# Kernel optimization log

Hardware: AMD Instinct MI355X
Metric: run time of the kernel (lower is better)

Reference implementation:

```python
import jax, jax.numpy as jnp
import numpy as np

N = 100000
E = 1600000
IN_DIM = 64
HID = 64
OUT = 64
BN_EPS = 1e-5


def setup_inputs() -> dict:
    key = jax.random.key(0)
    ks = jax.random.split(key, 16)
    x = jax.random.normal(ks[0], (N, IN_DIM), dtype=jnp.float32)
    edge_index = jax.random.randint(ks[1], (2, E), 0, N, dtype=jnp.int64)
    def lin(k, fan_in, fan_out):
        bound = 1.0 / np.sqrt(fan_in)
        kw, kb = jax.random.split(k)
        W = jax.random.uniform(kw, (fan_in, fan_out), jnp.float32, -bound, bound)
        b = jax.random.uniform(kb, (fan_out,), jnp.float32, -bound, bound)
        return W, b
    W1, b1 = lin(ks[2], IN_DIM, HID)
    W2, b2 = lin(ks[3], HID, HID)
    g1 = jnp.ones((HID,), jnp.float32)
    bt1 = jnp.zeros((HID,), jnp.float32)
    eps1 = jnp.zeros((), jnp.float32)
    W3, b3 = lin(ks[4], HID, HID)
    W4, b4 = lin(ks[5], HID, OUT)
    g2 = jnp.ones((OUT,), jnp.float32)
    bt2 = jnp.zeros((OUT,), jnp.float32)
    eps2 = jnp.zeros((), jnp.float32)
    return {"x": x, "edge_index": edge_index,
            "W1": W1, "b1": b1, "W2": W2, "b2": b2, "g1": g1, "bt1": bt1, "eps1": eps1,
            "W3": W3, "b3": b3, "W4": W4, "b4": b4, "g2": g2, "bt2": bt2, "eps2": eps2}


def _bn(h, gamma, beta):
    # BatchNorm1d in training mode: per-feature batch stats, biased variance
    mean = jnp.mean(h, axis=0)
    var = jnp.mean((h - mean) ** 2, axis=0)
    return (h - mean) * jax.lax.rsqrt(var + BN_EPS) * gamma + beta


def _gin_conv(x, src, dst, eps, Wa, ba, Wb, bb, gamma, beta):
    # scatter-add aggregation: sum_{j in N(i)} x_j
    agg = jax.ops.segment_sum(x[src], dst, num_segments=N)  # [N, D]
    h = (1.0 + eps) * x + agg
    h = jax.nn.relu(h @ Wa + ba)
    h = jax.nn.relu(h @ Wb + bb)
    return _bn(h, gamma, beta)


def reference(x, edge_index, W1, b1, W2, b2, g1, bt1, eps1, W3, b3, W4, b4, g2, bt2, eps2):
    src, dst = edge_index[0], edge_index[1]
    h = _gin_conv(x, src, dst, eps1, W1, b1, W2, b2, g1, bt1)
    h = _gin_conv(h, src, dst, eps2, W3, b3, W4, b4, g2, bt2)
    return (h, jax.nn.log_softmax(h, axis=-1))
```

## Files before the change

### kernel.cpp

```cpp
#include <hip/hip_runtime.h>

#define NN 100000
#define NE 1600000
#define NB 256
#define BSZ 391
#define EB 782

typedef __attribute__((ext_vector_type(8))) short short8;
typedef __attribute__((ext_vector_type(4))) float floatx4;

__device__ __forceinline__ unsigned short f2bf(float f) {
  unsigned u = __float_as_uint(f);
  u += 0x7fffu + ((u >> 16) & 1u);
  return (unsigned short)(u >> 16);
}
__device__ __forceinline__ float bf2f(unsigned short b) {
  return __uint_as_float(((unsigned)b) << 16);
}

__global__ __launch_bounds__(256) void k_cvtW(const float* __restrict__ W1,
                                              const float* __restrict__ W2,
                                              const float* __restrict__ W3,
                                              const float* __restrict__ W4,
                                              unsigned short* __restrict__ Wb) {
  int i = blockIdx.x * 256 + threadIdx.x;
  Wb[i] = f2bf(W1[i]);
  Wb[4096 + i] = f2bf(W2[i]);
  Wb[8192 + i] = f2bf(W3[i]);
  Wb[12288 + i] = f2bf(W4[i]);
}

__global__ __launch_bounds__(256) void k_phist(const int* __restrict__ dst,
                                               int* __restrict__ blockHist) {
  __shared__ int h[NB];
  h[threadIdx.x] = 0;
  __syncthreads();
  int base = blockIdx.x * 2048;
#pragma unroll
  for (int i = 0; i < 8; i++) {
    int e = base + i * 256 + threadIdx.x;
    if (e < NE) atomicAdd(&h[dst[e] / BSZ], 1);
  }
  __syncthreads();
  blockHist[blockIdx.x * NB + threadIdx.x] = h[threadIdx.x];
}

__global__ __launch_bounds__(1024) void k_colscan(const int* __restrict__ blockHist,
                                                  int* __restrict__ offsL,
                                                  int* __restrict__ colTot) {
  __shared__ int sh[1024];
  int c = blockIdx.x, t = threadIdx.x;
  int v = (t < EB) ? blockHist[t * NB + c] : 0;
  sh[t] = v;
  __syncthreads();
  for (int off = 1; off < 1024; off <<= 1) {
    int u = (t >= off) ? sh[t - off] : 0;
    __syncthreads();
    sh[t] += u;
    __syncthreads();
  }
  if (t < EB) offsL[t * NB + c] = sh[t] - v;
  if (t == EB - 1) colTot[c] = sh[t];
}

__global__ __launch_bounds__(256) void k_basescan(const int* __restrict__ colTot,
                                                  int* __restrict__ base) {
  __shared__ int sh[256];
  int t = threadIdx.x;
  int v = colTot[t];
  sh[t] = v;
  __syncthreads();
  for (int off = 1; off < 256; off <<= 1) {
    int u = (t >= off) ? sh[t - off] : 0;
    __syncthreads();
    sh[t] += u;
    __syncthreads();
  }
  base[t] = sh[t] - v;
  if (t == 255) base[256] = sh[255];
}

__global__ __launch_bounds__(256) void k_escat(const int* __restrict__ src,
                                               const int* __restrict__ dst,
                                               const int* __restrict__ offsL,
                                               const int* __restrict__ base,
                                               int2* __restrict__ ed) {
  __shared__ int h[NB];
  h[threadIdx.x] = 0;
  __syncthreads();
  int eb = blockIdx.x * 2048;
  const int* ofs = offsL + blockIdx.x * NB;
#pragma unroll
  for (int i = 0; i < 8; i++) {
    int e = eb + i * 256 + threadIdx.x;
    if (e < NE) {
      int d = dst[e];
      int c = d / BSZ;
      int r = atomicAdd(&h[c], 1);
      ed[base[c] + ofs[c] + r] = make_int2(src[e], d);
    }
  }
}

__global__ __launch_bounds__(256) void k_ellfill(const int2* __restrict__ ed,
                                                 const int* __restrict__ base,
                                                 int* __restrict__ ell,
                                                 int* __restrict__ deg) {
  __shared__ int cur[BSZ];
  int c = blockIdx.x;
  for (int i = threadIdx.x; i < BSZ; i += 256) cur[i] = 0;
  __syncthreads();
  int lo = base[c], hi = base[c + 1];
  int n0 = c * BSZ;
  for (int e = lo + threadIdx.x; e < hi; e += 256) {
    int2 sd = ed[e];
    int slot = atomicAdd(&cur[sd.y - n0], 1);
    if (slot < 64) ell[sd.y * 64 + slot] = sd.x;
  }
  __syncthreads();
  for (int i = threadIdx.x; i < BSZ; i += 256) {
    int n = n0 + i;
    if (n < NN) deg[n] = min(cur[i], 64);
  }
}

template <int MODE>
__global__ __launch_bounds__(256) void k_gather(const float* __restrict__ xf,
                                                const unsigned short* __restrict__ xb,
                                                const int* __restrict__ deg,
                                                const int* __restrict__ ell,
                                                const float* __restrict__ eps,
                                                const float* __restrict__ AB,
                                                unsigned short* __restrict__ agg) {
  const int lane = threadIdx.x & 31;
  const int slot = threadIdx.x >> 5;
  const int n = blockIdx.x * 8 + slot;
  const int fo = 2 * lane;
  float A0 = 1.0f, B0 = 0.0f, A1 = 1.0f, B1 = 0.0f;
  if (MODE) { A0 = AB[fo]; B0 = AB[64 + fo]; A1 = AB[fo + 1]; B1 = AB[64 + fo + 1]; }
  float s0, s1;
  if (MODE) {
    ushort2 u = *(const ushort2*)(xb + n * 64 + fo);
    s0 = fmaf(bf2f(u.x), A0, B0);
    s1 = fmaf(bf2f(u.y), A1, B1);
  } else {
    float2 u = *(const float2*)(xf + n * 64 + fo);
    s0 = u.x;
    s1 = u.y;
  }
  const float es = 1.0f + eps[0];
  float a0 = es * s0, a1 = es * s1;
  float b0 = 0, b1 = 0, c0 = 0, c1 = 0, d0 = 0, d1 = 0;
  const int cnt = deg[n];
  const int* row = ell + n * 64;
  const int4* r4 = (const int4*)row;
  int j = 0;
  for (; j + 4 <= cnt; j += 4) {
    int4 s4 = r4[j >> 2];
    if (MODE) {
      ushort2 u0 = *(const ushort2*)(xb + s4.x * 64 + fo);
      ushort2 u1 = *(const ushort2*)(xb + s4.y * 64 + fo);
      ushort2 u2 = *(const ushort2*)(xb + s4.z * 64 + fo);
      ushort2 u3 = *(const ushort2*)(xb + s4.w * 64 + fo);
      a0 = fmaf(bf2f(u0.x), A0, a0); a1 = fmaf(bf2f(u0.y), A1, a1);
      b0 = fmaf(bf2f(u1.x), A0, b0); b1 = fmaf(bf2f(u1.y), A1, b1);
      c0 = fmaf(bf2f(u2.x), A0, c0); c1 = fmaf(bf2f(u2.y), A1, c1);
      d0 = fmaf(bf2f(u3.x), A0, d0); d1 = fmaf(bf2f(u3.y), A1, d1);
      a0 += B0; a1 += B1; b0 += B0; b1 += B1;
      c0 += B0; c1 += B1; d0 += B0; d1 += B1;
    } else {
      float2 u0 = *(const float2*)(xf + s4.x * 64 + fo);
      float2 u1 = *(const float2*)(xf + s4.y * 64 + fo);
      float2 u2 = *(const float2*)(xf + s4.z * 64 + fo);
      float2 u3 = *(const float2*)(xf + s4.w * 64 + fo);
      a0 += u0.x; a1 += u0.y;
      b0 += u1.x; b1 += u1.y;
      c0 += u2.x; c1 += u2.y;
      d0 += u3.x; d1 += u3.y;
    }
  }
  for (; j < cnt; j++) {
    int s = row[j];
    if (MODE) {
      ushort2 u = *(const ushort2*)(xb + s * 64 + fo);
      a0 += fmaf(bf2f(u.x), A0, B0);
      a1 += fmaf(bf2f(u.y), A1, B1);
    } else {
      float2 u = *(const float2*)(xf + s * 64 + fo);
      a0 += u.x;
      a1 += u.y;
    }
  }
  float r0 = (a0 + b0) + (c0 + d0);
  float r1 = (a1 + b1) + (c1 + d1);
  ushort2 st;
  st.x = f2bf(r0);
  st.y = f2bf(r1);
  *(ushort2*)(agg + n * 64 + fo) = st;
}

__global__ __launch_bounds__(256) void k_mlp_mfma(
    const unsigned short* __restrict__ agg, const unsigned short* __restrict__ Wab,
    const float* __restrict__ ba, const float* __restrict__ bb,
    unsigned short* __restrict__ h2, double* __restrict__ stats) {
  const int l = threadIdx.x & 63;
  const int wv = threadIdx.x >> 6;
  const int l16 = l & 15, quad = l >> 4;

  short8 wfa[4][2], wfb[4][2];
#pragma unroll
  for (int c = 0; c < 4; c++)
#pragma unroll
    for (int t = 0; t < 2; t++)
#pragma unroll
      for (int j = 0; j < 8; j++) {
        int k = t * 32 + quad * 8 + j, nn = c * 16 + l16;
        wfa[c][t][j] = (short)Wab[k * 64 + nn];
        wfb[c][t][j] = (short)Wab[4096 + k * 64 + nn];
      }
  float bia[4], bib[4];
#pragma unroll
  for (int c = 0; c < 4; c++) { bia[c] = ba[c * 16 + l16]; bib[c] = bb[c * 16 + l16]; }

  __shared__ float Hs[4][16][68];
  __shared__ float sS[4][64], sQ[4][64];
  float ssum[4] = {0, 0, 0, 0}, ssq[4] = {0, 0, 0, 0};

  const int totw = gridDim.x * 4;
  for (int tile = blockIdx.x * 4 + wv; tile < NN / 16; tile += totw) {
    const int r0 = tile * 16;
    const unsigned short* ap = agg + (r0 + l16) * 64 + quad * 8;
    short8 a0 = *(const short8*)ap;
    short8 a1 = *(const short8*)(ap + 32);
#pragma unroll
    for (int c = 0; c < 4; c++) {
      floatx4 acc = {0.f, 0.f, 0.f, 0.f};
      acc = __builtin_amdgcn_mfma_f32_16x16x32_bf16(a0, wfa[c][0], acc, 0, 0, 0);
      acc = __builtin_amdgcn_mfma_f32_16x16x32_bf16(a1, wfa[c][1], acc, 0, 0, 0);
#pragma unroll
      for (int r = 0; r < 4; r++)
        Hs[wv][quad * 4 + r][c * 16 + l16] = fmaxf(acc[r] + bia[c], 0.0f);
    }
    short8 a20, a21;
#pragma unroll
    for (int j = 0; j < 8; j++) {
      a20[j] = (short)f2bf(Hs[wv][l16][quad * 8 + j]);
      a21[j] = (short)f2bf(Hs[wv][l16][32 + quad * 8 + j]);
    }
#pragma unroll
    for (int c = 0; c < 4; c++) {
      floatx4 acc = {0.f, 0.f, 0.f, 0.f};
      acc = __builtin_amdgcn_mfma_f32_16x16x32_bf16(a20, wfb[c][0], acc, 0, 0, 0);
      acc = __builtin_amdgcn_mfma_f32_16x16x32_bf16(a21, wfb[c][1], acc, 0, 0, 0);
#pragma unroll
      for (int r = 0; r < 4; r++) {
        float v = fmaxf(acc[r] + bib[c], 0.0f);
        h2[(r0 + quad * 4 + r) * 64 + c * 16 + l16] = f2bf(v);
        ssum[c] += v;
        ssq[c] += v * v;
      }
    }
  }
#pragma unroll
  for (int c = 0; c < 4; c++) {
    float s = ssum[c], q = ssq[c];
    s += __shfl_xor(s, 16, 64); s += __shfl_xor(s, 32, 64);
    q += __shfl_xor(q, 16, 64); q += __shfl_xor(q, 32, 64);
    if (quad == 0) { sS[wv][c * 16 + l16] = s; sQ[wv][c * 16 + l16] = q; }
  }
  __syncthreads();
  if (threadIdx.x < 64) {
    int ff = threadIdx.x;
    float s = sS[0][ff] + sS[1][ff] + sS[2][ff] + sS[3][ff];
    float q = sQ[0][ff] + sQ[1][ff] + sQ[2][ff] + sQ[3][ff];
    unsafeAtomicAdd(&stats[ff], (double)s);
    unsafeAtomicAdd(&stats[64 + ff], (double)q);
  }
}

__global__ void k_bnfin(const double* __restrict__ stats, const float* __restrict__ gam,
                        const float* __restrict__ bet, float* __restrict__ AB) {
  int f = threadIdx.x;
  double mean = stats[f] * (1.0 / NN);
  double var = stats[64 + f] * (1.0 / NN) - mean * mean;
  if (var < 0.0) var = 0.0;
  float rstd = (float)(1.0 / sqrt(var + 1e-5));
  float A = gam[f] * rstd;
  float B = bet[f] - (float)mean * A;
  AB[f] = A;
  AB[64 + f] = B;
}

__global__ __launch_bounds__(256) void k_out(const unsigned short* __restrict__ h2,
                                             const float* __restrict__ AB,
                                             float* __restrict__ out) {
  int f = threadIdx.x & 63;
  int n = blockIdx.x * 4 + (threadIdx.x >> 6);
  float v = bf2f(h2[n * 64 + f]);
  float h = fmaf(v, AB[f], AB[64 + f]);
  float m = h;
#pragma unroll
  for (int off = 32; off; off >>= 1) m = fmaxf(m, __shfl_xor(m, off, 64));
  float e = expf(h - m);
  float ssum = e;
#pragma unroll
  for (int off = 32; off; off >>= 1) ssum += __shfl_xor(ssum, off, 64);
  float lsm = (h - m) - logf(ssum);
  out[n * 64 + f] = h;
  out[(size_t)NN * 64 + n * 64 + f] = lsm;
}

extern "C" void kernel_launch(void* const* d_in, const int* in_sizes, int n_in,
                              void* d_out, int out_size, void* d_ws, size_t ws_size,
                              hipStream_t stream) {
  const float* x = (const float*)d_in[0];
  const int* ei = (const int*)d_in[1];
  const float* W1 = (const float*)d_in[2];
  const float* b1 = (const float*)d_in[3];
  const float* W2 = (const float*)d_in[4];
  const float* b2 = (const float*)d_in[5];
  const float* g1 = (const float*)d_in[6];
  const float* bt1 = (const float*)d_in[7];
  const float* e1 = (const float*)d_in[8];
  const float* W3 = (const float*)d_in[9];
  const float* b3 = (const float*)d_in[10];
  const float* W4 = (const float*)d_in[11];
  const float* b4 = (const float*)d_in[12];
  const float* g2 = (const float*)d_in[13];
  const float* bt2 = (const float*)d_in[14];
  const float* e2 = (const float*)d_in[15];
  const int* src = ei;
  const int* dst = ei + NE;

  char* ws = (char*)d_ws;
  unsigned short* aggb = (unsigned short*)(ws);
  unsigned short* h2b = (unsigned short*)(ws + 12800000);
  int* ell = (int*)(ws + 25600000);
  int2* ed = (int2*)(ws + 51200000);
  int* blockHist = (int*)(ws + 64000000);
  int* offsL = (int*)(ws + 64800768);
  int* colTot = (int*)(ws + 65601536);
  int* base = (int*)(ws + 65602560);
  int* deg = (int*)(ws + 65603600);
  double* st1 = (double*)(ws + 66003600);
  double* st2 = (double*)(ws + 66004624);
  float* AB1 = (float*)(ws + 66005648);
  float* AB2 = (float*)(ws + 66006160);
  unsigned short* Wbb = (unsigned short*)(ws + 66006672);
  float* out = (float*)d_out;

  hipMemsetAsync(ws + 66003600, 0, 2048, stream);

  k_cvtW<<<16, 256, 0, stream>>>(W1, W2, W3, W4, Wbb);

  k_phist<<<EB, 256, 0, stream>>>(dst, blockHist);
  k_colscan<<<NB, 1024, 0, stream>>>(blockHist, offsL, colTot);
  k_basescan<<<1, 256, 0, stream>>>(colTot, base);
  k_escat<<<EB, 256, 0, stream>>>(src, dst, offsL, base, ed);
  k_ellfill<<<NB, 256, 0, stream>>>(ed, base, ell, deg);

  k_gather<0><<<NN / 8, 256, 0, stream>>>(x, nullptr, deg, ell, e1, nullptr, aggb);
  k_mlp_mfma<<<391, 256, 0, stream>>>(aggb, Wbb, b1, b2, h2b, st1);
  k_bnfin<<<1, 64, 0, stream>>>(st1, g1, bt1, AB1);
  k_gather<1><<<NN / 8, 256, 0, stream>>>(nullptr, h2b, deg, ell, e2, AB1, aggb);
  k_mlp_mfma<<<391, 256, 0, stream>>>(aggb, Wbb + 8192, b3, b4, h2b, st2);
  k_bnfin<<<1, 64, 0, stream>>>(st2, g2, bt2, AB2);
  k_out<<<NN / 4, 256, 0, stream>>>(h2b, AB2, out);
}
```

Measured before the change: 314.0 us.

## Slice features into 8-wide column blocks and transpose ELL for cache-local gathers

Node features, aggregates and hidden activations are stored as 8 slices of 8 features each ([slice][node][8]). The gather kernel now uses one thread per node per slice, and reads neighbor indices from a transposed ELL table so those index loads coalesce across threads. Because each slice pass only touches a few MB of feature data, the random neighbor reads should mostly hit L2 or MALL instead of DRAM. The BatchNorm affine of layer one is folded algebraically into a single FMA at the end of the gather, and the MLP grid is doubled. The costs are an extra transpose kernel for x, reading each neighbor list eight times, and small 16–32 byte random accesses that may waste cache-line bandwidth.

```diff
diff --git a/kernel.cpp b/kernel.cpp
--- a/kernel.cpp
+++ b/kernel.cpp
@@ -104,7 +104,7 @@
 
 __global__ __launch_bounds__(256) void k_ellfill(const int2* __restrict__ ed,
                                                  const int* __restrict__ base,
-                                                 int* __restrict__ ell,
+                                                 int* __restrict__ ellT,
                                                  int* __restrict__ deg) {
   __shared__ int cur[BSZ];
   int c = blockIdx.x;
@@ -115,7 +115,7 @@
   for (int e = lo + threadIdx.x; e < hi; e += 256) {
     int2 sd = ed[e];
     int slot = atomicAdd(&cur[sd.y - n0], 1);
-    if (slot < 64) ell[sd.y * 64 + slot] = sd.x;
+    if (slot < 64) ellT[(size_t)slot * NN + sd.y] = sd.x;
   }
   __syncthreads();
   for (int i = threadIdx.x; i < BSZ; i += 256) {
@@ -124,79 +124,117 @@
   }
 }
 
+__global__ __launch_bounds__(256) void k_xpose(const float* __restrict__ x,
+                                               float* __restrict__ xs) {
+  int nl = threadIdx.x >> 3, s = threadIdx.x & 7;
+  int n = blockIdx.x * 32 + nl;
+  const floatx4* rp = (const floatx4*)(x + (size_t)n * 64 + s * 8);
+  floatx4 v0 = rp[0], v1 = rp[1];
+  floatx4* wp = (floatx4*)(xs + ((size_t)s * NN + n) * 8);
+  __builtin_nontemporal_store(v0, wp);
+  __builtin_nontemporal_store(v1, wp + 1);
+}
+
 template <int MODE>
-__global__ __launch_bounds__(256) void k_gather(const float* __restrict__ xf,
+__global__ __launch_bounds__(256) void k_gather(const float* __restrict__ xs,
                                                 const unsigned short* __restrict__ xb,
                                                 const int* __restrict__ deg,
-                                                const int* __restrict__ ell,
+                                                const int* __restrict__ ellT,
                                                 const float* __restrict__ eps,
                                                 const float* __restrict__ AB,
                                                 unsigned short* __restrict__ agg) {
-  const int lane = threadIdx.x & 31;
-  const int slot = threadIdx.x >> 5;
-  const int n = blockIdx.x * 8 + slot;
-  const int fo = 2 * lane;
-  float A0 = 1.0f, B0 = 0.0f, A1 = 1.0f, B1 = 0.0f;
-  if (MODE) { A0 = AB[fo]; B0 = AB[64 + fo]; A1 = AB[fo + 1]; B1 = AB[64 + fo + 1]; }
-  float s0, s1;
+  const int s = blockIdx.x & 7;
+  const int n = (blockIdx.x >> 3) * 256 + (int)threadIdx.x;
+  if (n >= NN) return;
+  const float es = 1.0f + eps[0];
+  const int cnt = __builtin_nontemporal_load(deg + n);
+  const size_t sbase = (size_t)s * NN;
+
+  float a0[8], a1[8];
+#pragma unroll
+  for (int i = 0; i < 8; i++) a1[i] = 0.0f;
+
   if (MODE) {
-    ushort2 u = *(const ushort2*)(xb + n * 64 + fo);
-    s0 = fmaf(bf2f(u.x), A0, B0);
-    s1 = fmaf(bf2f(u.y), A1, B1);
+    short8 v = *(const short8*)(xb + (sbase + n) * 8);
+#pragma unroll
+    for (int i = 0; i < 8; i++) a0[i] = es * bf2f((unsigned short)v[i]);
   } else {
-    float2 u = *(const float2*)(xf + n * 64 + fo);
-    s0 = u.x;
-    s1 = u.y;
-  }
-  const float es = 1.0f + eps[0];
-  float a0 = es * s0, a1 = es * s1;
-  float b0 = 0, b1 = 0, c0 = 0, c1 = 0, d0 = 0, d1 = 0;
-  const int cnt = deg[n];
-  const int* row = ell + n * 64;
-  const int4* r4 = (const int4*)row;
+    const floatx4* sp = (const floatx4*)(xs + (sbase + n) * 8);
+    floatx4 v0 = sp[0], v1 = sp[1];
+    a0[0] = es * v0.x; a0[1] = es * v0.y; a0[2] = es * v0.z; a0[3] = es * v0.w;
+    a0[4] = es * v1.x; a0[5] = es * v1.y; a0[6] = es * v1.z; a0[7] = es * v1.w;
+  }
+
+  const int* ep = ellT + n;
   int j = 0;
   for (; j + 4 <= cnt; j += 4) {
-    int4 s4 = r4[j >> 2];
+    int i0 = __builtin_nontemporal_load(ep + (size_t)(j + 0) * NN);
+    int i1 = __builtin_nontemporal_load(ep + (size_t)(j + 1) * NN);
+    int i2 = __builtin_nontemporal_load(ep + (size_t)(j + 2) * NN);
+    int i3 = __builtin_nontemporal_load(ep + (size_t)(j + 3) * NN);
     if (MODE) {
-      ushort2 u0 = *(const ushort2*)(xb + s4.x * 64 + fo);
-      ushort2 u1 = *(const ushort2*)(xb + s4.y * 64 + fo);
-      ushort2 u2 = *(const ushort2*)(xb + s4.z * 64 + fo);
-      ushort2 u3 = *(const ushort2*)(xb + s4.w * 64 + fo);
-      a0 = fmaf(bf2f(u0.x), A0, a0); a1 = fmaf(bf2f(u0.y), A1, a1);
-      b0 = fmaf(bf2f(u1.x), A0, b0); b1 = fmaf(bf2f(u1.y), A1, b1);
-      c0 = fmaf(bf2f(u2.x), A0, c0); c1 = fmaf(bf2f(u2.y), A1, c1);
-      d0 = fmaf(bf2f(u3.x), A0, d0); d1 = fmaf(bf2f(u3.y), A1, d1);
-      a0 += B0; a1 += B1; b0 += B0; b1 += B1;
-      c0 += B0; c1 += B1; d0 += B0; d1 += B1;
+      short8 u0 = *(const short8*)(xb + (sbase + i0) * 8);
+      short8 u1 = *(const short8*)(xb + (sbase + i1) * 8);
+      short8 u2 = *(const short8*)(xb + (sbase + i2) * 8);
+      short8 u3 = *(const short8*)(xb + (sbase + i3) * 8);
+#pragma unroll
+      for (int i = 0; i < 8; i++) {
+        a0[i] += bf2f((unsigned short)u0[i]) + bf2f((unsigned short)u1[i]);
+        a1[i] += bf2f((unsigned short)u2[i]) + bf2f((unsigned short)u3[i]);
+      }
     } else {
-      float2 u0 = *(const float2*)(xf + s4.x * 64 + fo);
-      float2 u1 = *(const float2*)(xf + s4.y * 64 + fo);
-      float2 u2 = *(const float2*)(xf + s4.z * 64 + fo);
-      float2 u3 = *(const float2*)(xf + s4.w * 64 + fo);
-      a0 += u0.x; a1 += u0.y;
-      b0 += u1.x; b1 += u1.y;
-      c0 += u2.x; c1 += u2.y;
-      d0 += u3.x; d1 += u3.y;
+      const floatx4* p0 = (const floatx4*)(xs + (sbase + i0) * 8);
+      const floatx4* p1 = (const floatx4*)(xs + (sbase + i1) * 8);
+      const floatx4* p2 = (const floatx4*)(xs + (sbase + i2) * 8);
+      const floatx4* p3 = (const floatx4*)(xs + (sbase + i3) * 8);
+      floatx4 q00 = p0[0], q01 = p0[1], q10 = p1[0], q11 = p1[1];
+      floatx4 q20 = p2[0], q21 = p2[1], q30 = p3[0], q31 = p3[1];
+      a0[0] += q00.x + q10.x; a0[1] += q00.y + q10.y;
+      a0[2] += q00.z + q10.z; a0[3] += q00.w + q10.w;
+      a0[4] += q01.x + q11.x; a0[5] += q01.y + q11.y;
+      a0[6] += q01.z + q11.z; a0[7] += q01.w + q11.w;
+      a1[0] += q20.x + q30.x; a1[1] += q20.y + q30.y;
+      a1[2] += q20.z + q30.z; a1[3] += q20.w + q30.w;
+      a1[4] += q21.x + q31.x; a1[5] += q21.y + q31.y;
+      a1[6] += q21.z + q31.z; a1[7] += q21.w + q31.w;
     }
   }
   for (; j < cnt; j++) {
-    int s = row[j];
+    int i0 = __builtin_nontemporal_load(ep + (size_t)j * NN);
     if (MODE) {
-      ushort2 u = *(const ushort2*)(xb + s * 64 + fo);
-      a0 += fmaf(bf2f(u.x), A0, B0);
-      a1 += fmaf(bf2f(u.y), A1, B1);
+      short8 u0 = *(const short8*)(xb + (sbase + i0) * 8);
+#pragma unroll
+      for (int i = 0; i < 8; i++) a0[i] += bf2f((unsigned short)u0[i]);
     } else {
-      float2 u = *(const float2*)(xf + s * 64 + fo);
-      a0 += u.x;
-      a1 += u.y;
-    }
-  }
-  float r0 = (a0 + b0) + (c0 + d0);
-  float r1 = (a1 + b1) + (c1 + d1);
-  ushort2 st;
-  st.x = f2bf(r0);
-  st.y = f2bf(r1);
-  *(ushort2*)(agg + n * 64 + fo) = st;
+      const floatx4* p0 = (const floatx4*)(xs + (sbase + i0) * 8);
+      floatx4 t0 = p0[0], t1 = p0[1];
+      a0[0] += t0.x; a0[1] += t0.y; a0[2] += t0.z; a0[3] += t0.w;
+      a0[4] += t1.x; a0[5] += t1.y; a0[6] += t1.z; a0[7] += t1.w;
+    }
+  }
+
+  float r[8];
+  if (MODE) {
+    const floatx4* Ap = (const floatx4*)(AB + s * 8);
+    const floatx4* Bp = (const floatx4*)(AB + 64 + s * 8);
+    floatx4 Aa = Ap[0], Ab = Ap[1], Ba = Bp[0], Bb = Bp[1];
+    float w = es + (float)cnt;
+    r[0] = fmaf(a0[0] + a1[0], Aa.x, w * Ba.x);
+    r[1] = fmaf(a0[1] + a1[1], Aa.y, w * Ba.y);
+    r[2] = fmaf(a0[2] + a1[2], Aa.z, w * Ba.z);
+    r[3] = fmaf(a0[3] + a1[3], Aa.w, w * Ba.w);
+    r[4] = fmaf(a0[4] + a1[4], Ab.x, w * Bb.x);
+    r[5] = fmaf(a0[5] + a1[5], Ab.y, w * Bb.y);
+    r[6] = fmaf(a0[6] + a1[6], Ab.z, w * Bb.z);
+    r[7] = fmaf(a0[7] + a1[7], Ab.w, w * Bb.w);
+  } else {
+#pragma unroll
+    for (int i = 0; i < 8; i++) r[i] = a0[i] + a1[i];
+  }
+  short8 st;
+#pragma unroll
+  for (int i = 0; i < 8; i++) st[i] = (short)f2bf(r[i]);
+  __builtin_nontemporal_store(st, (short8*)(agg + (sbase + n) * 8));
 }
 
 __global__ __launch_bounds__(256) void k_mlp_mfma(
@@ -229,9 +267,8 @@
   const int totw = gridDim.x * 4;
   for (int tile = blockIdx.x * 4 + wv; tile < NN / 16; tile += totw) {
     const int r0 = tile * 16;
-    const unsigned short* ap = agg + (r0 + l16) * 64 + quad * 8;
-    short8 a0 = *(const short8*)ap;
-    short8 a1 = *(const short8*)(ap + 32);
+    short8 a0 = *(const short8*)(agg + ((size_t)quad * NN + r0 + l16) * 8);
+    short8 a1 = *(const short8*)(agg + ((size_t)(4 + quad) * NN + r0 + l16) * 8);
 #pragma unroll
     for (int c = 0; c < 4; c++) {
       floatx4 acc = {0.f, 0.f, 0.f, 0.f};
@@ -252,10 +289,11 @@
       floatx4 acc = {0.f, 0.f, 0.f, 0.f};
       acc = __builtin_amdgcn_mfma_f32_16x16x32_bf16(a20, wfb[c][0], acc, 0, 0, 0);
       acc = __builtin_amdgcn_mfma_f32_16x16x32_bf16(a21, wfb[c][1], acc, 0, 0, 0);
+      int s2 = c * 2 + (l16 >> 3);
 #pragma unroll
       for (int r = 0; r < 4; r++) {
         float v = fmaxf(acc[r] + bib[c], 0.0f);
-        h2[(r0 + quad * 4 + r) * 64 + c * 16 + l16] = f2bf(v);
+        h2[((size_t)s2 * NN + (r0 + quad * 4 + r)) * 8 + (l16 & 7)] = f2bf(v);
         ssum[c] += v;
         ssq[c] += v * v;
       }
@@ -296,7 +334,7 @@
                                              float* __restrict__ out) {
   int f = threadIdx.x & 63;
   int n = blockIdx.x * 4 + (threadIdx.x >> 6);
-  float v = bf2f(h2[n * 64 + f]);
+  float v = bf2f(h2[((size_t)(f >> 3) * NN + n) * 8 + (f & 7)]);
   float h = fmaf(v, AB[f], AB[64 + f]);
   float m = h;
 #pragma unroll
@@ -334,8 +372,9 @@
 
   char* ws = (char*)d_ws;
   unsigned short* aggb = (unsigned short*)(ws);
-  unsigned short* h2b = (unsigned short*)(ws + 12800000);
-  int* ell = (int*)(ws + 25600000);
+  int* ellT = (int*)(ws + 12800000);
+  unsigned short* h2b = (unsigned short*)(ws + 38400000);
+  float* xs = (float*)(ws + 38400000);
   int2* ed = (int2*)(ws + 51200000);
   int* blockHist = (int*)(ws + 64000000);
   int* offsL = (int*)(ws + 64800768);
@@ -357,13 +396,15 @@
   k_colscan<<<NB, 1024, 0, stream>>>(blockHist, offsL, colTot);
   k_basescan<<<1, 256, 0, stream>>>(colTot, base);
   k_escat<<<EB, 256, 0, stream>>>(src, dst, offsL, base, ed);
-  k_ellfill<<<NB, 256, 0, stream>>>(ed, base, ell, deg);
-
-  k_gather<0><<<NN / 8, 256, 0, stream>>>(x, nullptr, deg, ell, e1, nullptr, aggb);
-  k_mlp_mfma<<<391, 256, 0, stream>>>(aggb, Wbb, b1, b2, h2b, st1);
+  k_ellfill<<<NB, 256, 0, stream>>>(ed, base, ellT, deg);
+
+  k_xpose<<<NN / 32, 256, 0, stream>>>(x, xs);
+
+  k_gather<0><<<8 * 391, 256, 0, stream>>>(xs, nullptr, deg, ellT, e1, nullptr, aggb);
+  k_mlp_mfma<<<782, 256, 0, stream>>>(aggb, Wbb, b1, b2, h2b, st1);
   k_bnfin<<<1, 64, 0, stream>>>(st1, g1, bt1, AB1);
-  k_gather<1><<<NN / 8, 256, 0, stream>>>(nullptr, h2b, deg, ell, e2, AB1, aggb);
-  k_mlp_mfma<<<391, 256, 0, stream>>>(aggb, Wbb + 8192, b3, b4, h2b, st2);
+  k_gather<1><<<8 * 391, 256, 0, stream>>>(nullptr, h2b, deg, ellT, e2, AB1, aggb);
+  k_mlp_mfma<<<782, 256, 0, stream>>>(aggb, Wbb + 8192, b3, b4, h2b, st2);
   k_bnfin<<<1, 64, 0, stream>>>(st2, g2, bt2, AB2);
   k_out<<<NN / 4, 256, 0, stream>>>(h2b, AB2, out);
 }
```

Measured after the change: 460.3 us. 1.47x slower.
